# Kernel optimization log

Measured on AMD Instinct MI355X. Metric: run time of the kernel, lower is better.

The kernel has to match this reference:

```python
import jax, jax.numpy as jnp
import numpy as np

N, E, D = 100000, 1600000, 128
BN_EPS = 1e-5


def setup_inputs() -> dict:
    key = jax.random.key(0)
    k0, k1, k2 = jax.random.split(key, 3)
    x = jax.random.normal(k0, (N, D), dtype=jnp.float32)
    edge_index = jax.random.randint(k1, (2, E), 0, N, dtype=jnp.int32)
    # GCNConv weight (glorot-ish scale) and bias
    W = jax.random.normal(k2, (D, D), dtype=jnp.float32) * (1.0 / np.sqrt(D))
    b = jnp.zeros((D,), dtype=jnp.float32)
    # BatchNorm1d affine params
    gamma = jnp.ones((D,), dtype=jnp.float32)
    beta = jnp.zeros((D,), dtype=jnp.float32)
    # PReLU single shared slope (torch default init 0.25)
    a_prelu = jnp.asarray(0.25, dtype=jnp.float32)
    return {"x": x, "W": W, "b": b, "gamma": gamma, "beta": beta,
            "a_prelu": a_prelu, "edge_index": edge_index}


def reference(x, W, b, gamma, beta, a_prelu, edge_index):
    n = x.shape[0]
    loops = jnp.arange(n, dtype=edge_index.dtype)
    src = jnp.concatenate([edge_index[0], loops])  # [E+N]
    dst = jnp.concatenate([edge_index[1], loops])  # [E+N]

    # GCN symmetric normalization with self-loops: deg counts incoming edges
    deg = jax.ops.segment_sum(jnp.ones_like(dst, dtype=x.dtype), dst, num_segments=n)
    dinv = jax.lax.rsqrt(deg)  # deg >= 1 thanks to self-loops
    enorm = dinv[src] * dinv[dst]  # [E+N]

    xw = x @ W                                        # [N, D] transform first
    msg = xw[src] * enorm[:, None]                    # gather + scale
    out = jax.ops.segment_sum(msg, dst, num_segments=n) + b  # scatter-add

    # BatchNorm1d over nodes (training-mode batch statistics, biased var)
    mean = jnp.mean(out, axis=0)
    var = jnp.mean(jnp.square(out - mean), axis=0)
    out = (out - mean) * jax.lax.rsqrt(var + BN_EPS) * gamma + beta

    # PReLU (single shared slope); dropout is identity in eval mode
    out = jnp.where(out > 0, out, a_prelu * out)

    # identity residual (in_dim == out_dim)
    return out + x
```

## Files before the change

### kernel.cpp

```cpp
#include <hip/hip_runtime.h>

#define DIM 128
#define BSH 8
#define BUCK 256
#define CAP2 6144
#define BINCH 2048
#define MAXB 1024
#define FPT 12

typedef __attribute__((ext_vector_type(8))) short bf16x8;
typedef __attribute__((ext_vector_type(4))) float f32x4;
union U8 { uint4 u; bf16x8 b; };

static __device__ __forceinline__ unsigned f2bf_bits(float f) {
  unsigned u = __float_as_uint(f);
  return (u + 0x7fffu + ((u >> 16) & 1u)) >> 16;
}
static __device__ __forceinline__ unsigned packbf(float a, float b) {
  return (f2bf_bits(a) & 0xffffu) | (f2bf_bits(b) << 16);
}
static __device__ __forceinline__ float bfu_lo(unsigned pk) { return __uint_as_float(pk << 16); }
static __device__ __forceinline__ float bfu_hi(unsigned pk) { return __uint_as_float(pk & 0xffff0000u); }

static __device__ __forceinline__ int eread(const int* __restrict__ e, long long idx, int fl64) {
  return fl64 ? e[idx * 2] : e[idx];
}

__global__ __launch_bounds__(256) void k_prep(const int* __restrict__ eidx, int E,
                                              int* __restrict__ bcnt,
                                              unsigned* __restrict__ tmp2, int nbuck,
                                              const float* __restrict__ W,
                                              unsigned* __restrict__ wbt,
                                              int NBB) {
  __shared__ int hist[MAXB];
  __shared__ int lcur[MAXB];
  __shared__ int sfl;
  int bid = blockIdx.x;
  int tid = threadIdx.x;

  if (bid < NBB) {
    if (tid < 64) {
      int w = eidx[tid * 2 + 1];
      unsigned long long m = __ballot(w == 0);
      if (tid == 0) sfl = (__popcll(m) >= 48) ? 1 : 0;
    }
    for (int i = tid; i < nbuck; i += 256) hist[i] = 0;
    __syncthreads();
    int fl = sfl;
    long long ebase = (long long)bid * BINCH;
    unsigned pk[BINCH / 256];
    int bb[BINCH / 256];
#pragma unroll
    for (int it = 0; it < BINCH / 256; ++it) {
      long long e = ebase + it * 256 + tid;
      bb[it] = -1;
      if (e < E) {
        int s = eread(eidx, e, fl);
        int d = eread(eidx, (long long)E + e, fl);
        bb[it] = d >> BSH;
        pk[it] = ((unsigned)s << BSH) | (unsigned)(d & (BUCK - 1));
        atomicAdd(&hist[bb[it]], 1);
      }
    }
    __syncthreads();
    for (int b = tid; b < nbuck; b += 256) {
      int h = hist[b];
      lcur[b] = h ? atomicAdd(&bcnt[b], h) : 0;
    }
    __syncthreads();
#pragma unroll
    for (int it = 0; it < BINCH / 256; ++it) {
      if (bb[it] >= 0) {
        int sl = atomicAdd(&lcur[bb[it]], 1);
        if (sl < CAP2) tmp2[(unsigned)bb[it] * CAP2 + sl] = pk[it];
      }
    }
  } else {
    int w = (bid - NBB) * 256 + tid;
    int c = w >> 6, kk = w & 63;
    float lo = W[(unsigned)(2 * kk) * DIM + c];
    float hi = W[(unsigned)(2 * kk + 1) * DIM + c];
    wbt[(unsigned)c * 64 + kk] = packbf(lo, hi);
  }
}

__global__ __launch_bounds__(512) void k_histsort(const int* __restrict__ bcnt,
                                                  unsigned* __restrict__ tmp2,
                                                  int* __restrict__ ofs2,
                                                  int* __restrict__ deg,
                                                  const float* __restrict__ x,
                                                  unsigned* __restrict__ xb, int n) {
  __shared__ unsigned srt[CAP2];
  __shared__ int hist[BUCK];
  __shared__ int sc2[BUCK];
  __shared__ int lcur[BUCK];
  __shared__ float dls[BUCK];
  int b = blockIdx.x, tid = threadIdx.x;
  int cnt = bcnt[b];
  if (cnt > CAP2) cnt = CAP2;
  unsigned base = (unsigned)b * CAP2;
  if (tid < BUCK) hist[tid] = 0;
  __syncthreads();
  unsigned r[FPT];
#pragma unroll
  for (int u = 0; u < FPT; ++u) {
    int j = u * 512 + tid;
    r[u] = 0xffffffffu;
    if (j < cnt) {
      r[u] = tmp2[base + j];
      atomicAdd(&hist[r[u] & (BUCK - 1)], 1);
    }
  }
  __syncthreads();
  if (tid < 64) {
    int h0 = hist[tid * 4], h1 = hist[tid * 4 + 1];
    int h2 = hist[tid * 4 + 2], h3 = hist[tid * 4 + 3];
    int s = h0 + h1 + h2 + h3;
    int pre = s;
#pragma unroll
    for (int d = 1; d < 64; d <<= 1) {
      int t = __shfl_up(pre, d);
      if (tid >= d) pre += t;
    }
    pre -= s;
    int e0 = pre, e1 = pre + h0, e2 = e1 + h1, e3 = e2 + h2;
    sc2[tid * 4] = e0;     lcur[tid * 4] = e0;
    sc2[tid * 4 + 1] = e1; lcur[tid * 4 + 1] = e1;
    sc2[tid * 4 + 2] = e2; lcur[tid * 4 + 2] = e2;
    sc2[tid * 4 + 3] = e3; lcur[tid * 4 + 3] = e3;
  }
  __syncthreads();
#pragma unroll
  for (int u = 0; u < FPT; ++u) {
    if (r[u] != 0xffffffffu) {
      int sl = atomicAdd(&lcur[r[u] & (BUCK - 1)], 1);
      srt[sl] = r[u];
    }
  }
  if (tid < BUCK) dls[tid] = rsqrtf((float)(hist[tid] + 1));
  __syncthreads();
#pragma unroll
  for (int u = 0; u < FPT; ++u) {
    int j = u * 512 + tid;
    if (j < cnt) tmp2[base + j] = srt[j];
  }
  if (tid < BUCK) {
    int node = b * BUCK + tid;
    if (node < n) {
      ofs2[node] = (int)base + sc2[tid];
      deg[node] = hist[tid];
    }
  }
  int nb0 = b * BUCK;
#pragma unroll
  for (int it = 0; it < 16; ++it) {
    int idx = it * 512 + tid;
    int ln = idx >> 5, p = idx & 31;
    int node = nb0 + ln;
    if (node < n) {
      float di = dls[ln];
      float4 v = *(const float4*)(x + (size_t)node * DIM + p * 4);
      uint2 o;
      o.x = packbf(v.x * di, v.y * di);
      o.y = packbf(v.z * di, v.w * di);
      *(uint2*)&xb[(unsigned)node * 64 + p * 2] = o;
    }
  }
}

__global__ __launch_bounds__(1024) void k_agemm(
    const unsigned* __restrict__ tmp2, const unsigned* __restrict__ xb,
    const int* __restrict__ ofs2, const int* __restrict__ deg,
    const unsigned* __restrict__ wbt, const float* __restrict__ bias,
    unsigned* __restrict__ preb, float* __restrict__ part, int n) {
  __shared__ unsigned SM[64 * 68 + 128 * 68];
  unsigned* As2 = SM;
  unsigned* WsT = SM + 64 * 68;
  __shared__ int nextn;
  int tid = threadIdx.x;
  int base = blockIdx.x * 64;
  int wv = tid >> 6, lane = tid & 63;

#pragma unroll
  for (int it = 0; it < 8; ++it) {
    int idx = it * 1024 + tid;
    WsT[(idx >> 6) * 68 + (idx & 63)] = wbt[idx];
  }
  if (tid == 0) nextn = 0;
  __syncthreads();

  for (;;) {
    int rr = 0;
    if (lane == 0) rr = atomicAdd(&nextn, 1);
    rr = __shfl(rr, 0);
    if (rr >= 64) break;
    int node = base + rr;
    float ax = 0.f, ay = 0.f, di = 1.f;
    if (node < n) {
      int dg = __builtin_amdgcn_readfirstlane(deg[node]);
      int e = __builtin_amdgcn_readfirstlane(ofs2[node]);
      di = rsqrtf((float)(dg + 1));
      unsigned xp = xb[(unsigned)node * 64 + lane];
      ax = bfu_lo(xp); ay = bfu_hi(xp);
      int e1 = e + dg;
      for (; e + 16 <= e1; e += 16) {
        unsigned s[16];
#pragma unroll
        for (int u = 0; u < 16; ++u) s[u] = tmp2[(unsigned)(e + u)] >> BSH;
        unsigned v[16];
#pragma unroll
        for (int u = 0; u < 16; ++u) v[u] = xb[s[u] * 64 + lane];
#pragma unroll
        for (int u = 0; u < 16; ++u) { ax += bfu_lo(v[u]); ay += bfu_hi(v[u]); }
      }
      for (; e + 4 <= e1; e += 4) {
        unsigned s0 = tmp2[(unsigned)e] >> BSH, s1 = tmp2[(unsigned)e + 1] >> BSH;
        unsigned s2 = tmp2[(unsigned)e + 2] >> BSH, s3 = tmp2[(unsigned)e + 3] >> BSH;
        unsigned v0 = xb[s0 * 64 + lane], v1 = xb[s1 * 64 + lane];
        unsigned v2 = xb[s2 * 64 + lane], v3 = xb[s3 * 64 + lane];
        ax += bfu_lo(v0); ay += bfu_hi(v0);
        ax += bfu_lo(v1); ay += bfu_hi(v1);
        ax += bfu_lo(v2); ay += bfu_hi(v2);
        ax += bfu_lo(v3); ay += bfu_hi(v3);
      }
      for (; e < e1; ++e) {
        unsigned vv = xb[(tmp2[(unsigned)e] >> BSH) * 64 + lane];
        ax += bfu_lo(vv); ay += bfu_hi(vv);
      }
    }
    As2[rr * 68 + lane] = packbf(ax * di, ay * di);
  }
  __syncthreads();

  int lg = lane >> 4, lr = lane & 15;
  int rt = wv & 3, ctb = (wv >> 2) * 2;
  f32x4 acc[2];
  acc[0] = (f32x4){0.f, 0.f, 0.f, 0.f};
  acc[1] = (f32x4){0.f, 0.f, 0.f, 0.f};
#pragma unroll
  for (int kt = 0; kt < 4; ++kt) {
    U8 bfr;
    bfr.u = *(const uint4*)&As2[(rt * 16 + lr) * 68 + kt * 16 + lg * 4];
#pragma unroll
    for (int t = 0; t < 2; ++t) {
      U8 afr;
      afr.u = *(const uint4*)&WsT[((ctb + t) * 16 + lr) * 68 + kt * 16 + lg * 4];
      acc[t] = __builtin_amdgcn_mfma_f32_16x16x32_bf16(afr.b, bfr.b, acc[t], 0, 0, 0);
    }
  }
  __syncthreads();

  float* Cf = (float*)SM;
#pragma unroll
  for (int t = 0; t < 2; ++t) {
    *(f32x4*)&Cf[(rt * 16 + lr) * 132 + (ctb + t) * 16 + lg * 4] = acc[t];
  }
  __syncthreads();

  float* bn = Cf + 64 * 132;
  int c2 = tid & 63, g4 = tid >> 6;
  float b0 = bias[2 * c2], b1 = bias[2 * c2 + 1];
  float cs0 = 0.f, cs1 = 0.f, cq0 = 0.f, cq1 = 0.f;
#pragma unroll
  for (int it = 0; it < 4; ++it) {
    int m = it * 16 + g4;
    int gg = base + m;
    float2 vv = *(const float2*)&Cf[m * 132 + 2 * c2];
    float v0 = vv.x + b0, v1 = vv.y + b1;
    if (gg < n) {
      preb[(unsigned)gg * 64 + c2] = packbf(v0, v1);
      cs0 += v0; cq0 += v0 * v0;
      cs1 += v1; cq1 += v1 * v1;
    }
  }
  bn[g4 * 256 + 2 * c2] = cs0;
  bn[g4 * 256 + 2 * c2 + 1] = cs1;
  bn[g4 * 256 + 128 + 2 * c2] = cq0;
  bn[g4 * 256 + 128 + 2 * c2 + 1] = cq1;
  __syncthreads();
  if (tid < 256) {
    float v = 0.f;
#pragma unroll
    for (int g = 0; g < 16; ++g) v += bn[g * 256 + tid];
    part[(size_t)blockIdx.x * 256 + tid] = v;
  }
}

__global__ __launch_bounds__(256) void k_redbn(const float* __restrict__ part, int nb,
                                               const float* __restrict__ gma,
                                               const float* __restrict__ bta,
                                               float* __restrict__ sc_,
                                               float* __restrict__ sh_, float invn) {
  __shared__ float r1[256], r2[256];
  int c = blockIdx.x, t = threadIdx.x;
  float s = 0.f, q = 0.f;
  for (int i = t; i < nb; i += 256) {
    s += part[(size_t)i * 256 + c];
    q += part[(size_t)i * 256 + 128 + c];
  }
  r1[t] = s; r2[t] = q;
  __syncthreads();
  for (int k = 128; k > 0; k >>= 1) {
    if (t < k) { r1[t] += r1[t + k]; r2[t] += r2[t + k]; }
    __syncthreads();
  }
  if (t == 0) {
    float mean = r1[0] * invn;
    float var = r2[0] * invn - mean * mean;
    float inv = rsqrtf(var + 1e-5f);
    float g = gma[c] * inv;
    sc_[c] = g;
    sh_[c] = bta[c] - mean * g;
  }
}

__global__ __launch_bounds__(256) void k_final(const unsigned* __restrict__ preb,
                                               const float* __restrict__ x,
                                               const float* __restrict__ sc,
                                               const float* __restrict__ sh,
                                               const float* __restrict__ apre,
                                               float* __restrict__ out, int n) {
  int t = blockIdx.x * 256 + threadIdx.x;
  int i = t >> 6, p = t & 63;
  if (i >= n) return;
  float a = apre[0];
  int c = p * 2;
  unsigned pk = preb[(unsigned)i * 64 + p];
  float t0 = bfu_lo(pk) * sc[c] + sh[c];
  float t1 = bfu_hi(pk) * sc[c + 1] + sh[c + 1];
  t0 = t0 > 0.f ? t0 : a * t0;
  t1 = t1 > 0.f ? t1 : a * t1;
  float2 xv = *(const float2*)(x + (size_t)i * DIM + c);
  t0 += xv.x;
  t1 += xv.y;
  *(float2*)(out + (size_t)i * DIM + c) = make_float2(t0, t1);
}

extern "C" void kernel_launch(void* const* d_in, const int* in_sizes, int n_in,
                              void* d_out, int out_size, void* d_ws, size_t ws_size,
                              hipStream_t stream) {
  (void)n_in; (void)out_size; (void)ws_size;
  const float* x    = (const float*)d_in[0];
  const float* W    = (const float*)d_in[1];
  const float* b    = (const float*)d_in[2];
  const float* gma  = (const float*)d_in[3];
  const float* bta  = (const float*)d_in[4];
  const float* apre = (const float*)d_in[5];
  const int* eidx   = (const int*)d_in[6];
  float* out        = (float*)d_out;

  const int N = in_sizes[0] / DIM;
  const int E = in_sizes[6] / 2;
  const int NB = (N + 63) / 64;
  const int NBUCK = (N + BUCK - 1) >> BSH;
  const int NBB = (E + BINCH - 1) / BINCH;
  const int NWT = 32;

  char* wsb = (char*)d_ws;
  size_t off_b = 0;
  auto take = [&](size_t bytes) -> void* {
    void* p = wsb + off_b;
    off_b += (bytes + 255) & ~(size_t)255;
    return p;
  };
  int*      bcnt  = (int*)     take((size_t)NBUCK * 4);
  int*      ofs2  = (int*)     take((size_t)N * 4);
  int*      deg   = (int*)     take((size_t)N * 4);
  unsigned* wbt   = (unsigned*)take((size_t)DIM * 64 * 4);
  unsigned* tmp2  = (unsigned*)take((size_t)NBUCK * CAP2 * 4);
  unsigned* xb    = (unsigned*)take((size_t)N * 64 * 4);
  unsigned* preb  = (unsigned*)take((size_t)N * 64 * 4);
  float*    part  = (float*)   take((size_t)NB * 256 * 4);
  float*    sc    = (float*)   take(DIM * 4);
  float*    sh    = (float*)   take(DIM * 4);

  hipMemsetAsync(bcnt, 0, (size_t)NBUCK * 4, stream);

  k_prep     <<<NBB + NWT, 256, 0, stream>>>(eidx, E, bcnt, tmp2, NBUCK, W, wbt, NBB);
  k_histsort <<<NBUCK, 512, 0, stream>>>(bcnt, tmp2, ofs2, deg, x, xb, N);
  k_agemm    <<<NB, 1024, 0, stream>>>(tmp2, xb, ofs2, deg, wbt, b, preb, part, N);
  k_redbn    <<<DIM, 256, 0, stream>>>(part, NB, gma, bta, sc, sh, 1.0f / (float)N);
  k_final    <<<(N * 64 + 255) / 256, 256, 0, stream>>>(preb, x, sc, sh, apre, out, N);
}
```

Baseline: 256.6 us.

## Shrink aggregate-GEMM blocks to 16 nodes and read W fragments from global

The fused aggregation+GEMM kernel now processes 16 nodes per 256-thread block instead of 64 nodes per 1024-thread block. The dynamic atomic work queue is replaced by a static four-nodes-per-wave assignment. W is no longer staged in shared memory; MFMA operands are loaded directly from global/L2. This cuts LDS use and sync scope and raises the number of resident blocks, but it quadruples the number of per-block BN partials that k_redbn must reduce and adds repeated global W reads.

```diff
diff --git a/kernel.cpp b/kernel.cpp
--- a/kernel.cpp
+++ b/kernel.cpp
@@ -7,6 +7,7 @@
 #define BINCH 2048
 #define MAXB 1024
 #define FPT 12
+#define NPB 16
 
 typedef __attribute__((ext_vector_type(8))) short bf16x8;
 typedef __attribute__((ext_vector_type(4))) float f32x4;
@@ -168,32 +169,20 @@
   }
 }
 
-__global__ __launch_bounds__(1024) void k_agemm(
+__global__ __launch_bounds__(256) void k_agemm(
     const unsigned* __restrict__ tmp2, const unsigned* __restrict__ xb,
     const int* __restrict__ ofs2, const int* __restrict__ deg,
     const unsigned* __restrict__ wbt, const float* __restrict__ bias,
     unsigned* __restrict__ preb, float* __restrict__ part, int n) {
-  __shared__ unsigned SM[64 * 68 + 128 * 68];
-  unsigned* As2 = SM;
-  unsigned* WsT = SM + 64 * 68;
-  __shared__ int nextn;
+  __shared__ float SM[NPB * 132 + 4 * 256];
+  unsigned* As2 = (unsigned*)SM;
   int tid = threadIdx.x;
-  int base = blockIdx.x * 64;
+  int base = blockIdx.x * NPB;
   int wv = tid >> 6, lane = tid & 63;
 
 #pragma unroll
-  for (int it = 0; it < 8; ++it) {
-    int idx = it * 1024 + tid;
-    WsT[(idx >> 6) * 68 + (idx & 63)] = wbt[idx];
-  }
-  if (tid == 0) nextn = 0;
-  __syncthreads();
-
-  for (;;) {
-    int rr = 0;
-    if (lane == 0) rr = atomicAdd(&nextn, 1);
-    rr = __shfl(rr, 0);
-    if (rr >= 64) break;
+  for (int i = 0; i < 4; ++i) {
+    int rr = wv * 4 + i;
     int node = base + rr;
     float ax = 0.f, ay = 0.f, di = 1.f;
     if (node < n) {
@@ -233,37 +222,36 @@
   __syncthreads();
 
   int lg = lane >> 4, lr = lane & 15;
-  int rt = wv & 3, ctb = (wv >> 2) * 2;
   f32x4 acc[2];
   acc[0] = (f32x4){0.f, 0.f, 0.f, 0.f};
   acc[1] = (f32x4){0.f, 0.f, 0.f, 0.f};
 #pragma unroll
   for (int kt = 0; kt < 4; ++kt) {
     U8 bfr;
-    bfr.u = *(const uint4*)&As2[(rt * 16 + lr) * 68 + kt * 16 + lg * 4];
+    bfr.u = *(const uint4*)&As2[lr * 68 + kt * 16 + lg * 4];
 #pragma unroll
     for (int t = 0; t < 2; ++t) {
       U8 afr;
-      afr.u = *(const uint4*)&WsT[((ctb + t) * 16 + lr) * 68 + kt * 16 + lg * 4];
+      afr.u = *(const uint4*)&wbt[((wv * 2 + t) * 16 + lr) * 64 + kt * 16 + lg * 4];
       acc[t] = __builtin_amdgcn_mfma_f32_16x16x32_bf16(afr.b, bfr.b, acc[t], 0, 0, 0);
     }
   }
   __syncthreads();
 
-  float* Cf = (float*)SM;
+  float* Cf = SM;
+  float* bn = SM + NPB * 132;
 #pragma unroll
   for (int t = 0; t < 2; ++t) {
-    *(f32x4*)&Cf[(rt * 16 + lr) * 132 + (ctb + t) * 16 + lg * 4] = acc[t];
-  }
-  __syncthreads();
-
-  float* bn = Cf + 64 * 132;
-  int c2 = tid & 63, g4 = tid >> 6;
+    *(f32x4*)&Cf[lr * 132 + (wv * 2 + t) * 16 + lg * 4] = acc[t];
+  }
+  __syncthreads();
+
+  int c2 = tid & 63, mg = tid >> 6;
   float b0 = bias[2 * c2], b1 = bias[2 * c2 + 1];
   float cs0 = 0.f, cs1 = 0.f, cq0 = 0.f, cq1 = 0.f;
 #pragma unroll
   for (int it = 0; it < 4; ++it) {
-    int m = it * 16 + g4;
+    int m = it * 4 + mg;
     int gg = base + m;
     float2 vv = *(const float2*)&Cf[m * 132 + 2 * c2];
     float v0 = vv.x + b0, v1 = vv.y + b1;
@@ -273,17 +261,12 @@
       cs1 += v1; cq1 += v1 * v1;
     }
   }
-  bn[g4 * 256 + 2 * c2] = cs0;
-  bn[g4 * 256 + 2 * c2 + 1] = cs1;
-  bn[g4 * 256 + 128 + 2 * c2] = cq0;
-  bn[g4 * 256 + 128 + 2 * c2 + 1] = cq1;
-  __syncthreads();
-  if (tid < 256) {
-    float v = 0.f;
-#pragma unroll
-    for (int g = 0; g < 16; ++g) v += bn[g * 256 + tid];
-    part[(size_t)blockIdx.x * 256 + tid] = v;
-  }
+  bn[mg * 256 + 2 * c2] = cs0;
+  bn[mg * 256 + 2 * c2 + 1] = cs1;
+  bn[mg * 256 + 128 + 2 * c2] = cq0;
+  bn[mg * 256 + 128 + 2 * c2 + 1] = cq1;
+  __syncthreads();
+  part[(size_t)blockIdx.x * 256 + tid] = bn[tid] + bn[256 + tid] + bn[512 + tid] + bn[768 + tid];
 }
 
 __global__ __launch_bounds__(256) void k_redbn(const float* __restrict__ part, int nb,
@@ -351,7 +334,7 @@
 
   const int N = in_sizes[0] / DIM;
   const int E = in_sizes[6] / 2;
-  const int NB = (N + 63) / 64;
+  const int NB = (N + NPB - 1) / NPB;
   const int NBUCK = (N + BUCK - 1) >> BSH;
   const int NBB = (E + BINCH - 1) / BINCH;
   const int NWT = 32;
@@ -378,7 +361,7 @@
 
   k_prep     <<<NBB + NWT, 256, 0, stream>>>(eidx, E, bcnt, tmp2, NBUCK, W, wbt, NBB);
   k_histsort <<<NBUCK, 512, 0, stream>>>(bcnt, tmp2, ofs2, deg, x, xb, N);
-  k_agemm    <<<NB, 1024, 0, stream>>>(tmp2, xb, ofs2, deg, wbt, b, preb, part, N);
+  k_agemm    <<<NB, 256, 0, stream>>>(tmp2, xb, ofs2, deg, wbt, b, preb, part, N);
   k_redbn    <<<DIM, 256, 0, stream>>>(part, NB, gma, bta, sc, sh, 1.0f / (float)N);
   k_final    <<<(N * 64 + 255) / 256, 256, 0, stream>>>(preb, x, sc, sh, apre, out, N);
 }
```

New measurement: 274.2 us. 1.07x slower.
